# Kernel optimization log

Hardware: AMD Instinct MI355X
Metric: run time of the kernel (lower is better)

The kernel has to match this reference:

```python
import jax, jax.numpy as jnp
import numpy as np

HEADS = 6
DIM_HEAD = 64
SCALE = DIM_HEAD ** -0.5
BN_EPS = 1e-5


def _dw_pw(x, w_dw, gamma, beta, mean, var, w_pw, stride):
    """Depthwise 3x3 conv (groups=C) -> BatchNorm (inference) -> 1x1 pointwise conv."""
    C = x.shape[1]
    y = jax.lax.conv_general_dilated(
        x, w_dw, window_strides=(stride, stride), padding=((1, 1), (1, 1)),
        dimension_numbers=('NCHW', 'OIHW', 'NCHW'), feature_group_count=C)
    inv = gamma / jnp.sqrt(var + BN_EPS)
    y = y * inv[None, :, None, None] + (beta - mean * inv)[None, :, None, None]
    # 1x1 conv as einsum: w_pw is [O, C]
    return jnp.einsum('bchw,oc->bohw', y, w_pw)


def setup_inputs() -> dict:
    key = jax.random.key(0)
    ks = jax.random.split(key, 10)
    B, C, H, W = 32, 384, 32, 32
    inner = HEADS * DIM_HEAD  # 384
    ws = 0.05  # weight scale to keep attention logits sane
    return {
        'x': jax.random.normal(ks[0], (B, C, H, W), jnp.float32),
        'q_dw': jax.random.normal(ks[1], (C, 1, 3, 3), jnp.float32) * ws,
        'q_gamma': jnp.ones((C,), jnp.float32),
        'q_beta': jnp.zeros((C,), jnp.float32),
        'q_mean': jax.random.normal(ks[2], (C,), jnp.float32) * 0.1,
        'q_var': jax.random.uniform(ks[3], (C,), jnp.float32) + 0.5,
        'q_pw': jax.random.normal(ks[4], (inner, C), jnp.float32) * ws,
        'kv_dw': jax.random.normal(ks[5], (C, 1, 3, 3), jnp.float32) * ws,
        'kv_gamma': jnp.ones((C,), jnp.float32),
        'kv_beta': jnp.zeros((C,), jnp.float32),
        'kv_mean': jax.random.normal(ks[6], (C,), jnp.float32) * 0.1,
        'kv_var': jax.random.uniform(ks[7], (C,), jnp.float32) + 0.5,
        'kv_pw': jax.random.normal(ks[8], (2 * inner, C), jnp.float32) * ws,
        'out_w': jax.random.normal(ks[9], (C, inner), jnp.float32) * ws,
        'out_b': jnp.zeros((C,), jnp.float32),
    }


def reference(x, q_dw, q_gamma, q_beta, q_mean, q_var, q_pw,
              kv_dw, kv_gamma, kv_beta, kv_mean, kv_var, kv_pw,
              out_w, out_b):
    B, C, H, W = x.shape
    h, d = HEADS, DIM_HEAD
    # Q at full resolution, K/V spatially downsampled (stride 2)
    q = _dw_pw(x, q_dw, q_gamma, q_beta, q_mean, q_var, q_pw, stride=1)   # [B, h*d, H, W]
    kv = _dw_pw(x, kv_dw, kv_gamma, kv_beta, kv_mean, kv_var, kv_pw, stride=2)  # [B, 2*h*d, Hk, Wk]
    k, v = jnp.split(kv, 2, axis=1)
    Hk, Wk = k.shape[2], k.shape[3]
    # 'b (h d) x y -> b h (x y) d'
    q = q.reshape(B, h, d, H * W).transpose(0, 1, 3, 2)
    k = k.reshape(B, h, d, Hk * Wk).transpose(0, 1, 3, 2)
    v = v.reshape(B, h, d, Hk * Wk).transpose(0, 1, 3, 2)
    dots = jnp.einsum('bhid,bhjd->bhij', q, k) * SCALE  # [B, h, HW, HkWk]
    attn = jax.nn.softmax(dots, axis=-1)
    out = jnp.einsum('bhij,bhjd->bhid', attn, v)        # [B, h, HW, d]
    # 'b h (x y) d -> b (h d) x y'
    out = out.transpose(0, 1, 3, 2).reshape(B, h * d, H, W)
    # final 1x1 conv projection (dropout is identity, p=0)
    return jnp.einsum('bchw,oc->bohw', out, out_w) + out_b[None, :, None, None]
```

## Files before the change

### kernel.cpp

```cpp
#include <hip/hip_runtime.h>
#include <hip/hip_bf16.h>

#define CIN 384
#define PQ 1024
#define PKV 256
#define HEADS 6
#define DH 64
#define INNER 384
#define ATTN_SCALE 0.125f

typedef __hip_bfloat16 bf16;
typedef unsigned short ushort;
typedef __bf16 bf16x8 __attribute__((ext_vector_type(8)));
typedef float floatx4 __attribute__((ext_vector_type(4)));

__device__ __forceinline__ float b2f(bf16 v) { return __bfloat162float(v); }
__device__ __forceinline__ bf16 f2b(float v) { return __float2bfloat16(v); }
__device__ __forceinline__ ushort f2bu(float v) { bf16 h = __float2bfloat16(v); return *(ushort*)&h; }
__device__ __forceinline__ float ldf(const void* p, size_t i, int isbf) {
    return isbf ? __bfloat162float(((const bf16*)p)[i]) : ((const float*)p)[i];
}
__device__ __forceinline__ void dma16(const bf16* g, bf16* l) {
    __builtin_amdgcn_global_load_lds(
        (const __attribute__((address_space(1))) unsigned int*)g,
        (__attribute__((address_space(3))) unsigned int*)l, 16, 0, 0);
}
__device__ __forceinline__ int probe_isbf(const void* x) {
    const unsigned* u = (const unsigned*)x;
    int cnt = 0;
    for (int i = 0; i < 64; i++) {
        unsigned e = (u[i] >> 7) & 0xFFu;
        cnt += (e >= 100u && e <= 140u) ? 1 : 0;
    }
    return cnt >= 48 ? 1 : 0;
}
__device__ __forceinline__ unsigned cvtpk(float lo, float hi) {
    unsigned r;
    asm("v_cvt_pk_bf16_f32 %0, %1, %2" : "=v"(r) : "v"(lo), "v"(hi));
    return r;
}
__device__ __forceinline__ void halfswap(unsigned a, unsigned b, unsigned& lo, unsigned& hi) {
#if __has_builtin(__builtin_amdgcn_permlane32_swap)
    auto r = __builtin_amdgcn_permlane32_swap(a, b, false, false);
    lo = r[0]; hi = r[1];
#else
    unsigned ax = (unsigned)__shfl_xor((int)a, 32, 64);
    unsigned bx = (unsigned)__shfl_xor((int)b, 32, 64);
    bool lower = (threadIdx.x & 32) == 0;
    lo = lower ? a : bx;
    hi = lower ? ax : b;
#endif
}

__global__ void wconv_kernel(const void* __restrict__ w0, const void* __restrict__ w1,
                             const void* __restrict__ w2, bf16* __restrict__ dst,
                             const void* __restrict__ xprobe) {
    int isbf = probe_isbf(xprobe);
    const int n0 = INNER * CIN, n1 = 2 * INNER * CIN, n2 = INNER * CIN;
    int i = blockIdx.x * 256 + threadIdx.x;
    int total = n0 + n1 + n2;
    for (; i < total; i += gridDim.x * 256) {
        float v;
        if (i < n0) v = ldf(w0, i, isbf);
        else if (i < n0 + n1) v = ldf(w1, i - n0, isbf);
        else v = ldf(w2, i - n0 - n1, isbf);
        dst[i] = f2b(v);
    }
}

template <int STRIDE, int HO, int WO>
__global__ __launch_bounds__(256) void dw_bn_kernel(
        const void* __restrict__ x, const void* __restrict__ wdw,
        const void* __restrict__ gamma, const void* __restrict__ beta,
        const void* __restrict__ mean, const void* __restrict__ var,
        bf16* __restrict__ yt) {
    constexpr int IN_ROWS = (8 - 1) * STRIDE + 3;
    constexpr int RL = 37;
    constexpr int PT = 8 * WO;
    constexpr unsigned XSZ = 32u * IN_ROWS * RL * 4;
    constexpr unsigned OSZ = (unsigned)PT * 40 * 2;
    __shared__ __align__(16) char smem[XSZ > OSZ ? XSZ : OSZ];
    float (*xin)[IN_ROWS][RL] = (float (*)[IN_ROWS][RL])smem;
    ushort (*outt)[40] = (ushort (*)[40])smem;

    int isbf = probe_isbf(x);
    int rg = blockIdx.x;
    int c0 = blockIdx.y * 32;
    int b  = blockIdx.z;
    int tid = threadIdx.x;
    int ri0 = rg * 8 * STRIDE - 1;

    for (int e = tid; e < 32 * IN_ROWS; e += 256) {
        int i = e % IN_ROWS, cc = e / IN_ROWS;
        xin[cc][i][0] = 0.f;
        xin[cc][i][33] = 0.f;
    }

    const int NCHUNK = 32 * IN_ROWS * 4;
    for (int ch = tid; ch < NCHUNK; ch += 256) {
        int wc = ch & 3;
        int t  = ch >> 2;
        int i  = t % IN_ROWS;
        int cc = t / IN_ROWS;
        int row = ri0 + i;
        float f[8];
        if (row >= 0 && row < 32) {
            size_t goff = ((size_t)(b * CIN + c0 + cc) * 32 + row) * 32 + wc * 8;
            if (isbf) {
                uint4 v = *(const uint4*)((const bf16*)x + goff);
                const ushort* u = (const ushort*)&v;
#pragma unroll
                for (int j = 0; j < 8; j++) f[j] = __uint_as_float((unsigned)u[j] << 16);
            } else {
                float4 v0 = *(const float4*)((const float*)x + goff);
                float4 v1 = *(const float4*)((const float*)x + goff + 4);
                f[0] = v0.x; f[1] = v0.y; f[2] = v0.z; f[3] = v0.w;
                f[4] = v1.x; f[5] = v1.y; f[6] = v1.z; f[7] = v1.w;
            }
        } else {
#pragma unroll
            for (int j = 0; j < 8; j++) f[j] = 0.f;
        }
        float* dst = &xin[cc][i][1 + wc * 8];
#pragma unroll
        for (int j = 0; j < 8; j++) dst[j] = f[j];
    }

    int cc = tid & 31;
    int g  = tid >> 5;
    int c  = c0 + cc;
    float w9[9];
#pragma unroll
    for (int k = 0; k < 9; k++) w9[k] = ldf(wdw, c * 9 + k, isbf);
    float inv  = ldf(gamma, c, isbf) * rsqrtf(ldf(var, c, isbf) + 1e-5f);
    float bias = ldf(beta, c, isbf) - ldf(mean, c, isbf) * inv;
    __syncthreads();

    const float* xr0 = xin[cc][g * STRIDE + 0];
    const float* xr1 = xin[cc][g * STRIDE + 1];
    const float* xr2 = xin[cc][g * STRIDE + 2];
    float o[WO];
    if (STRIDE == 1) {
        float a0 = xr0[0], a1 = xr0[1];
        float b0 = xr1[0], b1 = xr1[1];
        float q0 = xr2[0], q1 = xr2[1];
#pragma unroll
        for (int wo = 0; wo < WO; wo++) {
            float a2 = xr0[wo + 2], b2 = xr1[wo + 2], q2 = xr2[wo + 2];
            float acc = w9[0] * a0 + w9[1] * a1 + w9[2] * a2
                      + w9[3] * b0 + w9[4] * b1 + w9[5] * b2
                      + w9[6] * q0 + w9[7] * q1 + w9[8] * q2;
            o[wo] = acc * inv + bias;
            a0 = a1; a1 = a2; b0 = b1; b1 = b2; q0 = q1; q1 = q2;
        }
    } else {
        float a0 = xr0[0], b0 = xr1[0], q0 = xr2[0];
#pragma unroll
        for (int wo = 0; wo < WO; wo++) {
            float a1 = xr0[2 * wo + 1], a2 = xr0[2 * wo + 2];
            float b1 = xr1[2 * wo + 1], b2 = xr1[2 * wo + 2];
            float q1 = xr2[2 * wo + 1], q2 = xr2[2 * wo + 2];
            float acc = w9[0] * a0 + w9[1] * a1 + w9[2] * a2
                      + w9[3] * b0 + w9[4] * b1 + w9[5] * b2
                      + w9[6] * q0 + w9[7] * q1 + w9[8] * q2;
            o[wo] = acc * inv + bias;
            a0 = a2; b0 = b2; q0 = q2;
        }
    }
    __syncthreads();

#pragma unroll
    for (int wo = 0; wo < WO; wo++) outt[g * WO + wo][cc] = f2bu(o[wo]);
    __syncthreads();

    const size_t pbase = (size_t)b * (HO * WO) + (size_t)rg * 8 * WO;
    for (int chk = tid; chk < PT * 4; chk += 256) {
        int k = chk & 3, p = chk >> 2;
        uint4 v = *(const uint4*)&outt[p][k * 8];
        *(uint4*)(yt + (pbase + p) * CIN + c0 + k * 8) = v;
    }
}

template <int P, int MODE>
__global__ __launch_bounds__(256, 2) void mfma_pw(
        const bf16* __restrict__ wt, const bf16* __restrict__ yt,
        const void* __restrict__ bias, void* __restrict__ out0,
        bf16* __restrict__ out1, int O, const void* __restrict__ xprobe) {
    __shared__ __align__(16) bf16 As[2][8192];
    __shared__ __align__(16) bf16 Bs[2][8192];
    int tid = threadIdx.x;
    int wave = tid >> 6, lane = tid & 63;
    int l15 = lane & 15, quad = lane >> 4;
    int wm = wave & 1, wn = wave >> 1;
    int b = blockIdx.z;
    int p0 = blockIdx.x * 128;
    int o0 = blockIdx.y * 128;

    const bf16* asrc = yt + ((size_t)b * P + p0) * CIN;
    const bf16* bsrc = wt + (size_t)o0 * CIN;

    int srow = lane >> 3;
    int sc   = lane & 7;
    auto stage = [&](int step, int buf) {
#pragma unroll
        for (int it = 0; it < 4; it++) {
            int row = wave * 32 + it * 8 + srow;
            int g = sc ^ (row & 7);
            size_t goff = (size_t)row * CIN + step * 64 + g * 8;
            dma16(asrc + goff, &As[buf][(wave * 4 + it) * 512]);
            dma16(bsrc + goff, &Bs[buf][(wave * 4 + it) * 512]);
        }
    };

    floatx4 acc[4][4];
#pragma unroll
    for (int pt = 0; pt < 4; pt++)
#pragma unroll
        for (int ot = 0; ot < 4; ot++) acc[pt][ot] = (floatx4){0.f, 0.f, 0.f, 0.f};

    stage(0, 0);
    __syncthreads();
    for (int s = 0; s < CIN / 64; s++) {
        int buf = s & 1;
        if (s < CIN / 64 - 1) stage(s + 1, buf ^ 1);
#pragma unroll
        for (int ks = 0; ks < 2; ks++) {
            bf16x8 af[4], bw[4];
#pragma unroll
            for (int pt = 0; pt < 4; pt++) {
                int row = wm * 64 + pt * 16 + l15;
                af[pt] = *(const bf16x8*)&As[buf][row * 64 + (((ks * 4 + quad) ^ (row & 7))) * 8];
            }
#pragma unroll
            for (int ot = 0; ot < 4; ot++) {
                int row = wn * 64 + ot * 16 + l15;
                bw[ot] = *(const bf16x8*)&Bs[buf][row * 64 + (((ks * 4 + quad) ^ (row & 7))) * 8];
            }
#pragma unroll
            for (int pt = 0; pt < 4; pt++)
#pragma unroll
                for (int ot = 0; ot < 4; ot++)
                    acc[pt][ot] = __builtin_amdgcn_mfma_f32_16x16x32_bf16(af[pt], bw[ot], acc[pt][ot], 0, 0, 0);
        }
        __syncthreads();
    }

    int pw0 = p0 + wm * 64, ow0 = o0 + wn * 64;
    if (MODE == 2) {
        int isbf = probe_isbf(xprobe);
#pragma unroll
        for (int ot = 0; ot < 4; ot++) {
            int o = ow0 + ot * 16 + l15;
            float bv = ldf(bias, o, isbf);
#pragma unroll
            for (int pt = 0; pt < 4; pt++) {
                int p = pw0 + pt * 16 + quad * 4;
                size_t idx = ((size_t)b * O + o) * P + p;
                if (!isbf) {
                    float4 v4 = {acc[pt][ot][0] + bv, acc[pt][ot][1] + bv,
                                 acc[pt][ot][2] + bv, acc[pt][ot][3] + bv};
                    *(float4*)((float*)out0 + idx) = v4;
                } else {
                    ushort4 u4 = {f2bu(acc[pt][ot][0] + bv), f2bu(acc[pt][ot][1] + bv),
                                  f2bu(acc[pt][ot][2] + bv), f2bu(acc[pt][ot][3] + bv)};
                    *(ushort4*)((bf16*)out0 + idx) = u4;
                }
            }
        }
    } else if (MODE == 0) {
#pragma unroll
        for (int ot = 0; ot < 4; ot++) {
            int o = ow0 + ot * 16 + l15;
            int h = o >> 6, d = o & 63;
            bf16* base = (bf16*)out0 + ((size_t)(b * HEADS + h) * P) * 64 + d;
#pragma unroll
            for (int pt = 0; pt < 4; pt++)
#pragma unroll
                for (int r = 0; r < 4; r++)
                    base[(size_t)(pw0 + pt * 16 + quad * 4 + r) * 64] = f2b(acc[pt][ot][r]);
        }
    } else {
#pragma unroll
        for (int ot = 0; ot < 4; ot++) {
            int o = ow0 + ot * 16 + l15;
            if (o < INNER) {
                int h = o >> 6, d = o & 63;
                bf16* base = (bf16*)out0 + ((size_t)(b * HEADS + h) * P) * 64 + d;
#pragma unroll
                for (int pt = 0; pt < 4; pt++)
#pragma unroll
                    for (int r = 0; r < 4; r++)
                        base[(size_t)(pw0 + pt * 16 + quad * 4 + r) * 64] = f2b(acc[pt][ot][r]);
            } else {
                int ch = o - INNER;
                bf16* base = out1 + ((size_t)b * INNER + ch) * PKV;
#pragma unroll
                for (int pt = 0; pt < 4; pt++)
#pragma unroll
                    for (int r = 0; r < 4; r++)
                        base[pw0 + pt * 16 + quad * 4 + r] = f2b(acc[pt][ot][r]);
            }
        }
    }
}

__global__ __launch_bounds__(256, 3) void attn_kernel(
        const bf16* __restrict__ qalt, const bf16* __restrict__ kalt,
        const bf16* __restrict__ valt, bf16* __restrict__ ao) {
    __shared__ __align__(16) bf16 Vl[16384];
    __shared__ __align__(16) ushort Ot[4][16][80];
    int tid = threadIdx.x;
    int wave = tid >> 6, lane = tid & 63;
    int l15 = lane & 15, quad = lane >> 4;
    int blk = blockIdx.x;
    int swz = (blk & 7) * 192 + (blk >> 3);
    int seg = swz & 7;
    int bh  = swz >> 3;
    int b = bh / HEADS, h = bh % HEADS;

    const bf16* qbase = qalt + (size_t)(b * HEADS + h) * PQ * DH;
    const bf16* kbase = kalt + (size_t)(b * HEADS + h) * PKV * DH;
    const bf16* vbase = valt + ((size_t)b * INNER + h * DH) * PKV;

    {
        int d = lane >> 5, cs2 = lane & 31;
#pragma unroll
        for (int it = 0; it < 8; it++) {
            int dr = (wave * 8 + it) * 2 + d;
            int g = cs2 ^ (dr & 15);
            dma16(vbase + (size_t)dr * 256 + g * 8, &Vl[(wave * 8 + it) * 512]);
        }
    }

    int p0 = seg * 128 + wave * 16;
    const bf16* qrow = qbase + (size_t)(p0 + l15) * DH + quad * 8;
    const bf16* krow = kbase + (size_t)l15 * DH + quad * 8;
    bf16x8 qc0 = *(const bf16x8*)qrow;
    bf16x8 qc1 = *(const bf16x8*)(qrow + 32);

    const float C = ATTN_SCALE * 1.44269504f;

#pragma unroll
    for (int t = 0; t < 2; t++) {
        floatx4 s[16];
#pragma unroll
        for (int jt = 0; jt < 16; jt++) s[jt] = (floatx4){0.f, 0.f, 0.f, 0.f};
#pragma unroll
        for (int jt = 0; jt < 16; jt++) {
            bf16x8 k0 = *(const bf16x8*)(krow + jt * 16 * DH);
            bf16x8 k1 = *(const bf16x8*)(krow + jt * 16 * DH + 32);
            s[jt] = __builtin_amdgcn_mfma_f32_16x16x32_bf16(k0, qc0, s[jt], 0, 0, 0);
            s[jt] = __builtin_amdgcn_mfma_f32_16x16x32_bf16(k1, qc1, s[jt], 0, 0, 0);
        }

        bf16x8 qn0 = qc0, qn1 = qc1;
        if (t == 0) {
            qn0 = *(const bf16x8*)(qrow + 64 * DH);
            qn1 = *(const bf16x8*)(qrow + 64 * DH + 32);
        }

        float mx = s[0][0];
#pragma unroll
        for (int jt = 0; jt < 16; jt++)
#pragma unroll
            for (int r = 0; r < 4; r++) mx = fmaxf(mx, s[jt][r]);
        mx = fmaxf(mx, __shfl_xor(mx, 16, 64));
        mx = fmaxf(mx, __shfl_xor(mx, 32, 64));
        float mc = mx * C;
        float sm = 0.f;
#pragma unroll
        for (int jt = 0; jt < 16; jt++)
#pragma unroll
            for (int r = 0; r < 4; r++) {
                float e = exp2f(s[jt][r] * C - mc);
                s[jt][r] = e;
                sm += e;
            }
        sm += __shfl_xor(sm, 16, 64);
        sm += __shfl_xor(sm, 32, 64);
        float pinv = 1.f / sm;

        if (t == 0) __syncthreads();

        floatx4 oacc[4];
#pragma unroll
        for (int nt = 0; nt < 4; nt++) oacc[nt] = (floatx4){0.f, 0.f, 0.f, 0.f};
#pragma unroll
        for (int kk = 0; kk < 8; kk++) {
            floatx4 se = s[2 * kk], so = s[2 * kk + 1];
            unsigned E0 = cvtpk(se[0] * pinv, se[1] * pinv);
            unsigned E1 = cvtpk(se[2] * pinv, se[3] * pinv);
            unsigned D0 = cvtpk(so[0] * pinv, so[1] * pinv);
            unsigned D1 = cvtpk(so[2] * pinv, so[3] * pinv);
            unsigned lo0, hi0, lo1, hi1;
            halfswap(E0, D0, lo0, hi0);
            halfswap(E1, D1, lo1, hi1);
            unsigned sel0 = (quad & 1) ? hi0 : lo0;
            unsigned sel1 = (quad & 1) ? hi1 : lo1;
            unsigned x0 = (unsigned)__shfl_xor((int)sel0, 16, 64);
            unsigned x1 = (unsigned)__shfl_xor((int)sel1, 16, 64);
            union { unsigned u[4]; bf16x8 v; } pf;
            pf.u[0] = (quad & 1) ? x0 : sel0;
            pf.u[1] = (quad & 1) ? x1 : sel1;
            pf.u[2] = (quad & 1) ? sel0 : x0;
            pf.u[3] = (quad & 1) ? sel1 : x1;
#pragma unroll
            for (int nt = 0; nt < 4; nt++) {
                int d = nt * 16 + l15;
                bf16x8 bv = *(const bf16x8*)&Vl[d * 256 + ((kk * 4 + quad) ^ (d & 15)) * 8];
                oacc[nt] = __builtin_amdgcn_mfma_f32_16x16x32_bf16(pf.v, bv, oacc[nt], 0, 0, 0);
            }
        }

#pragma unroll
        for (int nt = 0; nt < 4; nt++)
#pragma unroll
            for (int r = 0; r < 4; r++)
                Ot[wave][quad * 4 + r][nt * 16 + l15] = f2bu(oacc[nt][r]);
        int row = lane >> 2, d0 = (lane & 3) * 16;
        uint4 ld0 = *(const uint4*)&Ot[wave][row][d0];
        uint4 ld1 = *(const uint4*)&Ot[wave][row][d0 + 8];
        bf16* dst = ao + ((size_t)b * PQ + p0 + t * 64 + row) * INNER + h * DH + d0;
        *(uint4*)dst = ld0;
        *(uint4*)(dst + 8) = ld1;

        qc0 = qn0; qc1 = qn1;
    }
}

extern "C" void kernel_launch(void* const* d_in, const int* in_sizes, int n_in,
                              void* d_out, int out_size, void* d_ws, size_t ws_size,
                              hipStream_t stream) {
    const void* x        = d_in[0];
    const void* q_dw     = d_in[1];
    const void* q_gamma  = d_in[2];
    const void* q_beta   = d_in[3];
    const void* q_mean   = d_in[4];
    const void* q_var    = d_in[5];
    const void* q_pw     = d_in[6];
    const void* kv_dw    = d_in[7];
    const void* kv_gamma = d_in[8];
    const void* kv_beta  = d_in[9];
    const void* kv_mean  = d_in[10];
    const void* kv_var   = d_in[11];
    const void* kv_pw    = d_in[12];
    const void* out_w    = d_in[13];
    const void* out_b    = d_in[14];

    bf16* pool = (bf16*)((char*)d_ws + 256);
    bf16* yqt  = pool;
    bf16* ykvt = yqt  + (size_t)32 * 1024 * 384;
    bf16* qalt = ykvt + (size_t)32 * 256 * 384;
    bf16* kalt = qalt + (size_t)32 * 6 * 1024 * 64;
    bf16* valt = kalt + (size_t)32 * 6 * 256 * 64;
    bf16* wbf  = valt + (size_t)32 * 384 * 256;
    bf16* qpw_bf = wbf;
    bf16* kvpw_bf = wbf + (size_t)INNER * CIN;
    bf16* outw_bf = kvpw_bf + (size_t)2 * INNER * CIN;
    bf16* aob  = yqt;

    wconv_kernel<<<576, 256, 0, stream>>>(q_pw, kv_pw, out_w, wbf, x);
    dw_bn_kernel<1, 32, 32><<<dim3(4, 12, 32), 256, 0, stream>>>(x, q_dw, q_gamma, q_beta, q_mean, q_var, yqt);
    dw_bn_kernel<2, 16, 16><<<dim3(2, 12, 32), 256, 0, stream>>>(x, kv_dw, kv_gamma, kv_beta, kv_mean, kv_var, ykvt);
    mfma_pw<1024, 0><<<dim3(8, 3, 32), 256, 0, stream>>>(qpw_bf, yqt, nullptr, qalt, nullptr, INNER, x);
    mfma_pw<256, 1><<<dim3(2, 6, 32), 256, 0, stream>>>(kvpw_bf, ykvt, nullptr, kalt, valt, 2 * INNER, x);
    attn_kernel<<<1536, 256, 0, stream>>>(qalt, kalt, valt, aob);
    mfma_pw<1024, 2><<<dim3(8, 3, 32), 256, 0, stream>>>(outw_bf, aob, out_b, d_out, nullptr, CIN, x);
}
```

Measured before the change: 263.5 us.

## Stage K in LDS with more query tiles per block; shrink pointwise GEMM K-step

The attention kernel now DMA-loads the whole per-head K tile into swizzled shared memory and has each block cover 256 queries (four tiles per wave) instead of 128, halving the grid. This removes repeated global K reads and amortizes the K/V load over more queries, at the cost of doubled LDS per block and occupancy lowered to 2 blocks. Separately, the pointwise MFMA GEMM uses a 32-wide K step with half-size LDS buffers and a 4-way swizzle, which means more pipeline iterations and barriers but less shared memory per block.

New measurement: 241.9 us. 8.2% less time.

```diff
diff --git a/kernel.cpp b/kernel.cpp
--- a/kernel.cpp
+++ b/kernel.cpp
@@ -186,8 +186,8 @@
         const bf16* __restrict__ wt, const bf16* __restrict__ yt,
         const void* __restrict__ bias, void* __restrict__ out0,
         bf16* __restrict__ out1, int O, const void* __restrict__ xprobe) {
-    __shared__ __align__(16) bf16 As[2][8192];
-    __shared__ __align__(16) bf16 Bs[2][8192];
+    __shared__ __align__(16) bf16 As[2][4096];
+    __shared__ __align__(16) bf16 Bs[2][4096];
     int tid = threadIdx.x;
     int wave = tid >> 6, lane = tid & 63;
     int l15 = lane & 15, quad = lane >> 4;
@@ -199,16 +199,16 @@
     const bf16* asrc = yt + ((size_t)b * P + p0) * CIN;
     const bf16* bsrc = wt + (size_t)o0 * CIN;
 
-    int srow = lane >> 3;
-    int sc   = lane & 7;
+    int srow = (lane >> 2);
+    int sc   = lane & 3;
     auto stage = [&](int step, int buf) {
 #pragma unroll
-        for (int it = 0; it < 4; it++) {
-            int row = wave * 32 + it * 8 + srow;
-            int g = sc ^ (row & 7);
-            size_t goff = (size_t)row * CIN + step * 64 + g * 8;
-            dma16(asrc + goff, &As[buf][(wave * 4 + it) * 512]);
-            dma16(bsrc + goff, &Bs[buf][(wave * 4 + it) * 512]);
+        for (int it = 0; it < 2; it++) {
+            int row = wave * 32 + it * 16 + srow;
+            int g = sc ^ (row & 3);
+            size_t goff = (size_t)row * CIN + step * 32 + g * 8;
+            dma16(asrc + goff, &As[buf][(wave * 2 + it) * 512]);
+            dma16(bsrc + goff, &Bs[buf][(wave * 2 + it) * 512]);
         }
     };
 
@@ -220,28 +220,22 @@
 
     stage(0, 0);
     __syncthreads();
-    for (int s = 0; s < CIN / 64; s++) {
+    for (int s = 0; s < CIN / 32; s++) {
         int buf = s & 1;
-        if (s < CIN / 64 - 1) stage(s + 1, buf ^ 1);
-#pragma unroll
-        for (int ks = 0; ks < 2; ks++) {
-            bf16x8 af[4], bw[4];
-#pragma unroll
-            for (int pt = 0; pt < 4; pt++) {
-                int row = wm * 64 + pt * 16 + l15;
-                af[pt] = *(const bf16x8*)&As[buf][row * 64 + (((ks * 4 + quad) ^ (row & 7))) * 8];
-            }
-#pragma unroll
-            for (int ot = 0; ot < 4; ot++) {
-                int row = wn * 64 + ot * 16 + l15;
-                bw[ot] = *(const bf16x8*)&Bs[buf][row * 64 + (((ks * 4 + quad) ^ (row & 7))) * 8];
-            }
-#pragma unroll
-            for (int pt = 0; pt < 4; pt++)
-#pragma unroll
-                for (int ot = 0; ot < 4; ot++)
-                    acc[pt][ot] = __builtin_amdgcn_mfma_f32_16x16x32_bf16(af[pt], bw[ot], acc[pt][ot], 0, 0, 0);
-        }
+        if (s < CIN / 32 - 1) stage(s + 1, buf ^ 1);
+        bf16x8 af[4], bw[4];
+        int slot = (quad ^ (l15 & 3)) * 8;
+#pragma unroll
+        for (int pt = 0; pt < 4; pt++)
+            af[pt] = *(const bf16x8*)&As[buf][(wm * 64 + pt * 16 + l15) * 32 + slot];
+#pragma unroll
+        for (int ot = 0; ot < 4; ot++)
+            bw[ot] = *(const bf16x8*)&Bs[buf][(wn * 64 + ot * 16 + l15) * 32 + slot];
+#pragma unroll
+        for (int pt = 0; pt < 4; pt++)
+#pragma unroll
+            for (int ot = 0; ot < 4; ot++)
+                acc[pt][ot] = __builtin_amdgcn_mfma_f32_16x16x32_bf16(af[pt], bw[ot], acc[pt][ot], 0, 0, 0);
         __syncthreads();
     }
 
@@ -304,18 +298,19 @@
     }
 }
 
-__global__ __launch_bounds__(256, 3) void attn_kernel(
+__global__ __launch_bounds__(256, 2) void attn_kernel(
         const bf16* __restrict__ qalt, const bf16* __restrict__ kalt,
         const bf16* __restrict__ valt, bf16* __restrict__ ao) {
+    __shared__ __align__(16) bf16 Kl[16384];
     __shared__ __align__(16) bf16 Vl[16384];
     __shared__ __align__(16) ushort Ot[4][16][80];
     int tid = threadIdx.x;
     int wave = tid >> 6, lane = tid & 63;
     int l15 = lane & 15, quad = lane >> 4;
     int blk = blockIdx.x;
-    int swz = (blk & 7) * 192 + (blk >> 3);
-    int seg = swz & 7;
-    int bh  = swz >> 3;
+    int swz = (blk & 7) * 96 + (blk >> 3);
+    int seg = swz & 3;
+    int bh  = swz >> 2;
     int b = bh / HEADS, h = bh % HEADS;
 
     const bf16* qbase = qalt + (size_t)(b * HEADS + h) * PQ * DH;
@@ -323,6 +318,13 @@
     const bf16* vbase = valt + ((size_t)b * INNER + h * DH) * PKV;
 
     {
+        int j = lane >> 3, cs = lane & 7;
+#pragma unroll
+        for (int it = 0; it < 8; it++) {
+            int jr = (wave * 8 + it) * 8 + j;
+            int g = cs ^ (jr & 7);
+            dma16(kbase + (size_t)jr * 64 + g * 8, &Kl[(wave * 8 + it) * 512]);
+        }
         int d = lane >> 5, cs2 = lane & 31;
 #pragma unroll
         for (int it = 0; it < 8; it++) {
@@ -332,31 +334,33 @@
         }
     }
 
-    int p0 = seg * 128 + wave * 16;
+    int p0 = seg * 256 + wave * 16;
     const bf16* qrow = qbase + (size_t)(p0 + l15) * DH + quad * 8;
-    const bf16* krow = kbase + (size_t)l15 * DH + quad * 8;
     bf16x8 qc0 = *(const bf16x8*)qrow;
     bf16x8 qc1 = *(const bf16x8*)(qrow + 32);
+    __syncthreads();
 
     const float C = ATTN_SCALE * 1.44269504f;
 
 #pragma unroll
-    for (int t = 0; t < 2; t++) {
+    for (int t = 0; t < 4; t++) {
+        bf16x8 qn0 = qc0, qn1 = qc1;
+        if (t < 3) {
+            const bf16* qr = qrow + (size_t)(t + 1) * 64 * DH;
+            qn0 = *(const bf16x8*)qr;
+            qn1 = *(const bf16x8*)(qr + 32);
+        }
+
         floatx4 s[16];
 #pragma unroll
         for (int jt = 0; jt < 16; jt++) s[jt] = (floatx4){0.f, 0.f, 0.f, 0.f};
 #pragma unroll
         for (int jt = 0; jt < 16; jt++) {
-            bf16x8 k0 = *(const bf16x8*)(krow + jt * 16 * DH);
-            bf16x8 k1 = *(const bf16x8*)(krow + jt * 16 * DH + 32);
+            int j = jt * 16 + l15;
+            bf16x8 k0 = *(const bf16x8*)&Kl[j * 64 + (quad ^ (j & 7)) * 8];
+            bf16x8 k1 = *(const bf16x8*)&Kl[j * 64 + ((4 + quad) ^ (j & 7)) * 8];
             s[jt] = __builtin_amdgcn_mfma_f32_16x16x32_bf16(k0, qc0, s[jt], 0, 0, 0);
             s[jt] = __builtin_amdgcn_mfma_f32_16x16x32_bf16(k1, qc1, s[jt], 0, 0, 0);
-        }
-
-        bf16x8 qn0 = qc0, qn1 = qc1;
-        if (t == 0) {
-            qn0 = *(const bf16x8*)(qrow + 64 * DH);
-            qn1 = *(const bf16x8*)(qrow + 64 * DH + 32);
         }
 
         float mx = s[0][0];
@@ -379,8 +383,6 @@
         sm += __shfl_xor(sm, 16, 64);
         sm += __shfl_xor(sm, 32, 64);
         float pinv = 1.f / sm;
-
-        if (t == 0) __syncthreads();
 
         floatx4 oacc[4];
 #pragma unroll
@@ -464,6 +466,6 @@
     dw_bn_kernel<2, 16, 16><<<dim3(2, 12, 32), 256, 0, stream>>>(x, kv_dw, kv_gamma, kv_beta, kv_mean, kv_var, ykvt);
     mfma_pw<1024, 0><<<dim3(8, 3, 32), 256, 0, stream>>>(qpw_bf, yqt, nullptr, qalt, nullptr, INNER, x);
     mfma_pw<256, 1><<<dim3(2, 6, 32), 256, 0, stream>>>(kvpw_bf, ykvt, nullptr, kalt, valt, 2 * INNER, x);
-    attn_kernel<<<1536, 256, 0, stream>>>(qalt, kalt, valt, aob);
+    attn_kernel<<<768, 256, 0, stream>>>(qalt, kalt, valt, aob);
     mfma_pw<1024, 2><<<dim3(8, 3, 32), 256, 0, stream>>>(outw_bf, aob, out_b, d_out, nullptr, CIN, x);
 }
```
